# Performance work log

Hardware: AMD Instinct MI355X
Metric: run time of the kernel (lower is better)

## Reference

```python
import jax, jax.numpy as jnp
import numpy as np

DIM = 1024
HEADS = 16
SCALE = DIM ** -0.5  # NOTE: original uses full dim, not head dim


def setup_inputs() -> dict:
    key = jax.random.key(0)
    k1, k2, k3, k4 = jax.random.split(key, 4)
    x = jax.random.normal(k1, (2, 2048, DIM), dtype=jnp.float32)
    # torch nn.Linear(dim, 3*dim, bias=False): y = x @ W_qkv (stored here as [dim, 3*dim])
    w_qkv = jax.random.normal(k2, (DIM, 3 * DIM), dtype=jnp.float32) * (DIM ** -0.5)
    w_out = jax.random.normal(k3, (DIM, DIM), dtype=jnp.float32) * (DIM ** -0.5)
    b_out = jax.random.normal(k4, (DIM,), dtype=jnp.float32) * 0.01
    return {"x": x, "w_qkv": w_qkv, "w_out": w_out, "b_out": b_out}


def reference(x, w_qkv, w_out, b_out):
    b, n, d = x.shape
    h = HEADS
    hd = d // h
    qkv = x @ w_qkv  # [b, n, 3*d]
    # last dim layout is (qkv, h, hd) per rearrange 'b n (qkv h d) -> qkv b h n d'
    qkv = qkv.reshape(b, n, 3, h, hd)
    q, k, v = (jnp.moveaxis(qkv, (2, 3), (0, 2))[i] for i in range(3))  # each [b, h, n, hd]
    dots = jnp.einsum('bhid,bhjd->bhij', q, k) * SCALE
    causal_mask = jnp.triu(jnp.ones((n, n), dtype=bool), k=1)
    dots = jnp.where(causal_mask, -jnp.inf, dots)
    attn = jax.nn.softmax(dots, axis=-1)
    out = jnp.einsum('bhij,bhjd->bhid', attn, v)
    out = jnp.moveaxis(out, 1, 2).reshape(b, n, d)  # 'b h n d -> b n (h d)'
    return out @ w_out + b_out
```

## Files before the change

kernel.cpp:

```cpp
#include <hip/hip_runtime.h>

typedef __attribute__((ext_vector_type(8))) short bf16x8;
typedef __attribute__((ext_vector_type(4))) float f32x4;
typedef unsigned short u16;
typedef unsigned int u32;

#define SEQ 2048
#define NHEAD 16
#define EXP2_SCALE 0.045084219f

__device__ __forceinline__ u16 f2bf(float f){
  u32 u = __builtin_bit_cast(u32, f);
  u += 0x7FFFu + ((u >> 16) & 1u);
  return (u16)(u >> 16);
}

__device__ __forceinline__ void gl16(const u16* g, u16* l){
  __builtin_amdgcn_global_load_lds(
      (__attribute__((address_space(1))) void*)(unsigned long long)(const void*)g,
      (__attribute__((address_space(3))) void*)(unsigned)(unsigned long long)(const void*)l,
      16, 0, 0);
}

__global__ __launch_bounds__(256) void prep(const float* __restrict__ x,
                                            const float* __restrict__ w_qkv,
                                            const float* __restrict__ w_out,
                                            u16* __restrict__ xb,
                                            u16* __restrict__ wqkvT,
                                            u16* __restrict__ woutT){
  __shared__ u16 t[32][33];
  const int bid = blockIdx.x;
  if (bid < 4096){
    int i = (bid * 256 + threadIdx.x) << 2;
    float4 v = *(const float4*)&x[i];
    ushort4 o;
    o.x = f2bf(v.x); o.y = f2bf(v.y); o.z = f2bf(v.z); o.w = f2bf(v.w);
    *(ushort4*)&xb[i] = o;
    return;
  }
  const float* src; u16* dst; int R, C, bx, by;
  if (bid < 7168){ int tt = bid - 4096; src = w_qkv; dst = wqkvT; R = 1024; C = 3072; bx = tt % 96; by = tt / 96; }
  else           { int tt = bid - 7168; src = w_out; dst = woutT; R = 1024; C = 1024; bx = tt % 32; by = tt / 32; }
  const int c0 = bx << 5, r0 = by << 5;
  const int tx = threadIdx.x & 31, tg = threadIdx.x >> 5;
  #pragma unroll
  for (int i = 0; i < 4; i++){
    int r = (tg << 2) + i;
    t[r][tx] = f2bf(src[(size_t)(r0 + r) * C + (c0 + tx)]);
  }
  __syncthreads();
  #pragma unroll
  for (int i = 0; i < 4; i++){
    int c = (tg << 2) + i;
    dst[(size_t)(c0 + c) * R + (r0 + tx)] = t[tx][c];
  }
}

__device__ __forceinline__ int sw32(int row, int c){
  return row * 32 + (((c ^ ((row >> 1) & 3))) << 3);
}

__global__ __launch_bounds__(256) void gemm_qkv(const u16* __restrict__ A,
                                                const u16* __restrict__ Bt,
                                                u16* __restrict__ Qo,
                                                u16* __restrict__ Ko,
                                                u16* __restrict__ Vto){
  __shared__ u16 As[128 * 32];
  __shared__ u16 Bs[128 * 32];
  const int tid = threadIdx.x;
  const int lane = tid & 63, wid = tid >> 6;
  const int l15 = lane & 15, quad = lane >> 4;
  const int wm = wid >> 1, wn = wid & 1;
  const int bm = blockIdx.y << 7, bn = blockIdx.x << 7;
  const int qkv_idx = bn >> 10;

  const int rT = wid * 32 + (lane >> 2);
  const int cT = (lane & 3) ^ ((rT >> 1) & 3);
  const u16* gA0 = A  + (size_t)(bm + rT) * 1024 + cT * 8;
  const u16* gB0 = Bt + (size_t)(bn + rT) * 1024 + cT * 8;
  u16* lA0 = &As[wid * 1024];
  u16* lB0 = &Bs[wid * 1024];

  f32x4 acc[4][4];
  #pragma unroll
  for (int i = 0; i < 4; i++)
    #pragma unroll
    for (int j = 0; j < 4; j++) acc[i][j] = (f32x4){0.f, 0.f, 0.f, 0.f};

  if (qkv_idx != 2){
    for (int k0 = 0; k0 < 1024; k0 += 32){
      gl16(gA0 + k0,            lA0);
      gl16(gA0 + k0 + 16*1024,  lA0 + 512);
      gl16(gB0 + k0,            lB0);
      gl16(gB0 + k0 + 16*1024,  lB0 + 512);
      __syncthreads();
      bf16x8 af[4], bfr[4];
      #pragma unroll
      for (int mt = 0; mt < 4; mt++)
        af[mt] = *(const bf16x8*)&As[sw32(wm * 64 + mt * 16 + l15, quad)];
      #pragma unroll
      for (int nt = 0; nt < 4; nt++)
        bfr[nt] = *(const bf16x8*)&Bs[sw32(wn * 64 + nt * 16 + l15, quad)];
      #pragma unroll
      for (int mt = 0; mt < 4; mt++)
        #pragma unroll
        for (int nt = 0; nt < 4; nt++)
          acc[mt][nt] = __builtin_amdgcn_mfma_f32_16x16x32_bf16(af[mt], bfr[nt], acc[mt][nt], 0, 0, 0);
      __syncthreads();
    }
    const float qscale = (qkv_idx == 0) ? EXP2_SCALE : 1.0f;
    #pragma unroll
    for (int mt = 0; mt < 4; mt++){
      #pragma unroll
      for (int nt = 0; nt < 4; nt++){
        int col = bn + wn * 64 + nt * 16 + l15;
        int head = (col & 1023) >> 6, hd_i = col & 63;
        #pragma unroll
        for (int r = 0; r < 4; r++){
          int row = bm + wm * 64 + mt * 16 + quad * 4 + r;
          int b = row >> 11, pos = row & 2047;
          size_t bh = ((size_t)(b * NHEAD + head)) << 17;
          u16 v = f2bf(acc[mt][nt][r] * qscale);
          if (qkv_idx == 0) Qo[bh + ((size_t)pos << 6) + hd_i] = v;
          else              Ko[bh + ((size_t)pos << 6) + hd_i] = v;
        }
      }
    }
  } else {
    for (int k0 = 0; k0 < 1024; k0 += 32){
      gl16(gA0 + k0,            lA0);
      gl16(gA0 + k0 + 16*1024,  lA0 + 512);
      gl16(gB0 + k0,            lB0);
      gl16(gB0 + k0 + 16*1024,  lB0 + 512);
      __syncthreads();
      bf16x8 af[4], bfr[4];
      #pragma unroll
      for (int mt = 0; mt < 4; mt++)
        af[mt] = *(const bf16x8*)&As[sw32(wm * 64 + mt * 16 + l15, quad)];
      #pragma unroll
      for (int nt = 0; nt < 4; nt++)
        bfr[nt] = *(const bf16x8*)&Bs[sw32(wn * 64 + nt * 16 + l15, quad)];
      #pragma unroll
      for (int mt = 0; mt < 4; mt++)
        #pragma unroll
        for (int nt = 0; nt < 4; nt++)
          acc[mt][nt] = __builtin_amdgcn_mfma_f32_16x16x32_bf16(bfr[nt], af[mt], acc[mt][nt], 0, 0, 0);
      __syncthreads();
    }
    #pragma unroll
    for (int mt = 0; mt < 4; mt++){
      int row_m = bm + wm * 64 + mt * 16 + l15;
      int b = row_m >> 11, pos = row_m & 2047;
      #pragma unroll
      for (int nt = 0; nt < 4; nt++){
        #pragma unroll
        for (int r = 0; r < 4; r++){
          int c = bn + wn * 64 + nt * 16 + quad * 4 + r;
          int head = (c & 1023) >> 6, hd_i = c & 63;
          size_t bh = ((size_t)(b * NHEAD + head)) << 17;
          Vto[bh + ((size_t)hd_i << 11) + pos] = f2bf(acc[mt][nt][r]);
        }
      }
    }
  }
}

__global__ __launch_bounds__(256) void attn_kernel(const u16* __restrict__ Q,
                                                   const u16* __restrict__ K,
                                                   const u16* __restrict__ Vt,
                                                   u16* __restrict__ Oo){
  __shared__ u16 Ks[128 * 64];
  __shared__ u16 Vts[64 * 128];
  __shared__ u16 Ps[4][16 * 136];
  const int tid = threadIdx.x;
  const int lane = tid & 63, wid = tid >> 6;
  const int l15 = lane & 15, quad = lane >> 4;
  const int bh = blockIdx.x & 31;
  const int qt = 31 - (blockIdx.x >> 5);
  const size_t base = ((size_t)bh) << 17;
  const int b = bh >> 4, h = bh & 15;

  const u16* qsrc = Q + base + ((size_t)((qt << 6) + wid * 16 + l15) << 6) + quad * 8;
  const bf16x8 bq0 = *(const bf16x8*)qsrc;
  const bf16x8 bq1 = *(const bf16x8*)(qsrc + 32);

  const int rK = wid * 32 + (lane >> 3);
  const int cK = (lane & 7) ^ (rK & 7);
  const u16* gK0 = K + base + ((size_t)rK << 6) + cK * 8;
  u16* lK = &Ks[wid * 4 * 512];
  const u16* gV[4];
  #pragma unroll
  for (int t = 0; t < 4; t++){
    int rv = wid * 16 + t * 4 + (lane >> 4);
    int cv = (lane & 15) ^ (rv & 15);
    gV[t] = Vt + base + (size_t)rv * 2048 + cv * 8;
  }
  u16* lV = &Vts[wid * 4 * 512];

  f32x4 o[4];
  #pragma unroll
  for (int dt = 0; dt < 4; dt++) o[dt] = (f32x4){0.f, 0.f, 0.f, 0.f};
  float l = 0.f;
  const int qpos = (qt << 6) + wid * 16 + l15;
  const int jt_max = qt >> 1;
  u16* Pw = &Ps[wid][0];

  for (int jt = 0; jt <= jt_max; jt++){
    const u16* gk = gK0 + (size_t)jt * 8192;
    #pragma unroll
    for (int t = 0; t < 4; t++) gl16(gk + t * 512, lK + t * 512);
    #pragma unroll
    for (int t = 0; t < 4; t++) gl16(gV[t] + (jt << 7), lV + t * 512);
    __syncthreads();

    f32x4 st[8];
    #pragma unroll
    for (int mt = 0; mt < 8; mt++) st[mt] = (f32x4){0.f, 0.f, 0.f, 0.f};
    #pragma unroll
    for (int mt = 0; mt < 8; mt++){
      int kvr = mt * 16 + l15;
      bf16x8 ak0 = *(const bf16x8*)&Ks[kvr * 64 + ((quad ^ (kvr & 7)) << 3)];
      st[mt] = __builtin_amdgcn_mfma_f32_16x16x32_bf16(ak0, bq0, st[mt], 0, 0, 0);
      bf16x8 ak1 = *(const bf16x8*)&Ks[kvr * 64 + (((4 + quad) ^ (kvr & 7)) << 3)];
      st[mt] = __builtin_amdgcn_mfma_f32_16x16x32_bf16(ak1, bq1, st[mt], 0, 0, 0);
    }

    const bool diag = (jt == jt_max);
    float rs = 0.f;
    #pragma unroll
    for (int mt = 0; mt < 8; mt++){
      float pr[4];
      #pragma unroll
      for (int r = 0; r < 4; r++){
        float w = st[mt][r];
        if (diag){
          int kv = (jt << 7) + mt * 16 + quad * 4 + r;
          if (kv > qpos) w = -INFINITY;
        }
        pr[r] = __builtin_amdgcn_exp2f(w);
      }
      rs += (pr[0] + pr[1]) + (pr[2] + pr[3]);
      u32 a0 = __builtin_bit_cast(u32, pr[0]) + 0x8000u;
      u32 a1 = __builtin_bit_cast(u32, pr[1]) + 0x8000u;
      u32 a2 = __builtin_bit_cast(u32, pr[2]) + 0x8000u;
      u32 a3 = __builtin_bit_cast(u32, pr[3]) + 0x8000u;
      uint2 pk;
      pk.x = __builtin_amdgcn_perm(a1, a0, 0x07060302u);
      pk.y = __builtin_amdgcn_perm(a3, a2, 0x07060302u);
      *(uint2*)&Pw[l15 * 136 + mt * 16 + quad * 4] = pk;
    }
    rs += __shfl_xor(rs, 16);
    rs += __shfl_xor(rs, 32);
    l += rs;

    #pragma unroll
    for (int ks = 0; ks < 4; ks++){
      bf16x8 bp = *(const bf16x8*)&Pw[l15 * 136 + ks * 32 + quad * 8];
      #pragma unroll
      for (int dt = 0; dt < 4; dt++){
        int dr = dt * 16 + l15;
        bf16x8 av = *(const bf16x8*)&Vts[dr * 128 + (((ks * 4 + quad) ^ (dr & 15)) << 3)];
        o[dt] = __builtin_amdgcn_mfma_f32_16x16x32_bf16(av, bp, o[dt], 0, 0, 0);
      }
    }
    __syncthreads();
  }

  float inv = 1.f / l;
  const size_t orow = (size_t)((b << 11) + qpos) * 1024 + h * 64;
  #pragma unroll
  for (int dt = 0; dt < 4; dt++){
    ushort4 w;
    w.x = f2bf(o[dt][0] * inv); w.y = f2bf(o[dt][1] * inv);
    w.z = f2bf(o[dt][2] * inv); w.w = f2bf(o[dt][3] * inv);
    *(ushort4*)&Oo[orow + dt * 16 + quad * 4] = w;
  }
}

__global__ __launch_bounds__(256) void gemm_out(const u16* __restrict__ A,
                                                const u16* __restrict__ Bt,
                                                const float* __restrict__ bias,
                                                float* __restrict__ out){
  __shared__ u16 As[128 * 32];
  __shared__ u16 Bs[128 * 32];
  const int tid = threadIdx.x;
  const int lane = tid & 63, wid = tid >> 6;
  const int l15 = lane & 15, quad = lane >> 4;
  const int wm = wid >> 1, wn = wid & 1;
  const int bm = blockIdx.y << 7, bn = blockIdx.x << 7;

  const int rT = wid * 32 + (lane >> 2);
  const int cT = (lane & 3) ^ ((rT >> 1) & 3);
  const u16* gA0 = A  + (size_t)(bm + rT) * 1024 + cT * 8;
  const u16* gB0 = Bt + (size_t)(bn + rT) * 1024 + cT * 8;
  u16* lA0 = &As[wid * 1024];
  u16* lB0 = &Bs[wid * 1024];

  f32x4 acc[4][4];
  #pragma unroll
  for (int i = 0; i < 4; i++)
    #pragma unroll
    for (int j = 0; j < 4; j++) acc[i][j] = (f32x4){0.f, 0.f, 0.f, 0.f};

  for (int k0 = 0; k0 < 1024; k0 += 32){
    gl16(gA0 + k0,            lA0);
    gl16(gA0 + k0 + 16*1024,  lA0 + 512);
    gl16(gB0 + k0,            lB0);
    gl16(gB0 + k0 + 16*1024,  lB0 + 512);
    __syncthreads();

    bf16x8 af[4], bfr[4];
    #pragma unroll
    for (int mt = 0; mt < 4; mt++)
      af[mt] = *(const bf16x8*)&As[sw32(wm * 64 + mt * 16 + l15, quad)];
    #pragma unroll
    for (int nt = 0; nt < 4; nt++)
      bfr[nt] = *(const bf16x8*)&Bs[sw32(wn * 64 + nt * 16 + l15, quad)];
    #pragma unroll
    for (int mt = 0; mt < 4; mt++)
      #pragma unroll
      for (int nt = 0; nt < 4; nt++)
        acc[mt][nt] = __builtin_amdgcn_mfma_f32_16x16x32_bf16(af[mt], bfr[nt], acc[mt][nt], 0, 0, 0);
    __syncthreads();
  }

  #pragma unroll
  for (int nt = 0; nt < 4; nt++){
    int col = bn + wn * 64 + nt * 16 + l15;
    float bv = bias[col];
    #pragma unroll
    for (int mt = 0; mt < 4; mt++)
      #pragma unroll
      for (int r = 0; r < 4; r++){
        int row = bm + wm * 64 + mt * 16 + quad * 4 + r;
        out[(size_t)row * 1024 + col] = acc[mt][nt][r] + bv;
      }
  }
}

extern "C" void kernel_launch(void* const* d_in, const int* in_sizes, int n_in,
                              void* d_out, int out_size, void* d_ws, size_t ws_size,
                              hipStream_t stream){
  const float* x     = (const float*)d_in[0];
  const float* w_qkv = (const float*)d_in[1];
  const float* w_out = (const float*)d_in[2];
  const float* b_out = (const float*)d_in[3];
  float* out = (float*)d_out;

  char* ws = (char*)d_ws;
  u16* xb    = (u16*)(ws);
  u16* wqkvT = (u16*)(ws + (8u  << 20));
  u16* woutT = (u16*)(ws + (14u << 20));
  u16* Qb    = (u16*)(ws + (16u << 20));
  u16* Kb    = (u16*)(ws + (24u << 20));
  u16* Vtb   = (u16*)(ws + (32u << 20));
  u16* attn  = (u16*)(ws + (40u << 20));

  prep<<<8192, 256, 0, stream>>>(x, w_qkv, w_out, xb, wqkvT, woutT);
  gemm_qkv<<<dim3(24, 32), 256, 0, stream>>>(xb, wqkvT, Qb, Kb, Vtb);
  attn_kernel<<<dim3(1024), 256, 0, stream>>>(Qb, Kb, Vtb, attn);
  gemm_out<<<dim3(8, 32), 256, 0, stream>>>(attn, woutT, b_out, out);
}
```

Baseline: 177.6 us.

## Double GEMM K-tile to 64 and process two Q tiles per attention block

Both GEMMs now stage a 64-wide K slice per iteration with a new XOR swizzle. That halves the number of barriers and global-to-LDS rounds per output tile, and the two V-branch loops are merged into one. The attention kernel gives each block 128 query rows, as two 64-row sub-tiles, so each K/V tile loaded into LDS is reused twice, and it launches half as many blocks. In exchange, LDS use per GEMM block doubles, register pressure in attention rises, and attention has fewer blocks to spread across CUs, with coarser causal load balancing.

```diff
diff --git a/kernel.cpp b/kernel.cpp
--- a/kernel.cpp
+++ b/kernel.cpp
@@ -56,17 +56,13 @@
   }
 }
 
-__device__ __forceinline__ int sw32(int row, int c){
-  return row * 32 + (((c ^ ((row >> 1) & 3))) << 3);
-}
-
 __global__ __launch_bounds__(256) void gemm_qkv(const u16* __restrict__ A,
                                                 const u16* __restrict__ Bt,
                                                 u16* __restrict__ Qo,
                                                 u16* __restrict__ Ko,
                                                 u16* __restrict__ Vto){
-  __shared__ u16 As[128 * 32];
-  __shared__ u16 Bs[128 * 32];
+  __shared__ u16 As[128 * 64];
+  __shared__ u16 Bs[128 * 64];
   const int tid = threadIdx.x;
   const int lane = tid & 63, wid = tid >> 6;
   const int l15 = lane & 15, quad = lane >> 4;
@@ -74,12 +70,12 @@
   const int bm = blockIdx.y << 7, bn = blockIdx.x << 7;
   const int qkv_idx = bn >> 10;
 
-  const int rT = wid * 32 + (lane >> 2);
-  const int cT = (lane & 3) ^ ((rT >> 1) & 3);
-  const u16* gA0 = A  + (size_t)(bm + rT) * 1024 + cT * 8;
-  const u16* gB0 = Bt + (size_t)(bn + rT) * 1024 + cT * 8;
-  u16* lA0 = &As[wid * 1024];
-  u16* lB0 = &Bs[wid * 1024];
+  const int lr = lane >> 3;
+  const int cc = (lane & 7) ^ lr;
+  const u16* gA0 = A  + (size_t)(bm + wid * 32 + lr) * 1024 + (cc << 3);
+  const u16* gB0 = Bt + (size_t)(bn + wid * 32 + lr) * 1024 + (cc << 3);
+  u16* lA0 = &As[wid * 2048];
+  u16* lB0 = &Bs[wid * 2048];
 
   f32x4 acc[4][4];
   #pragma unroll
@@ -87,27 +83,45 @@
     #pragma unroll
     for (int j = 0; j < 4; j++) acc[i][j] = (f32x4){0.f, 0.f, 0.f, 0.f};
 
-  if (qkv_idx != 2){
-    for (int k0 = 0; k0 < 1024; k0 += 32){
-      gl16(gA0 + k0,            lA0);
-      gl16(gA0 + k0 + 16*1024,  lA0 + 512);
-      gl16(gB0 + k0,            lB0);
-      gl16(gB0 + k0 + 16*1024,  lB0 + 512);
-      __syncthreads();
+  const bool vbranch = (qkv_idx == 2);
+  for (int k0 = 0; k0 < 1024; k0 += 64){
+    #pragma unroll
+    for (int t = 0; t < 4; t++){
+      gl16(gA0 + k0 + t * 8192, lA0 + t * 512);
+      gl16(gB0 + k0 + t * 8192, lB0 + t * 512);
+    }
+    __syncthreads();
+    #pragma unroll
+    for (int hf = 0; hf < 2; hf++){
       bf16x8 af[4], bfr[4];
       #pragma unroll
-      for (int mt = 0; mt < 4; mt++)
-        af[mt] = *(const bf16x8*)&As[sw32(wm * 64 + mt * 16 + l15, quad)];
-      #pragma unroll
-      for (int nt = 0; nt < 4; nt++)
-        bfr[nt] = *(const bf16x8*)&Bs[sw32(wn * 64 + nt * 16 + l15, quad)];
-      #pragma unroll
-      for (int mt = 0; mt < 4; mt++)
-        #pragma unroll
-        for (int nt = 0; nt < 4; nt++)
-          acc[mt][nt] = __builtin_amdgcn_mfma_f32_16x16x32_bf16(af[mt], bfr[nt], acc[mt][nt], 0, 0, 0);
-      __syncthreads();
-    }
+      for (int mt = 0; mt < 4; mt++){
+        int row = wm * 64 + mt * 16 + l15;
+        af[mt] = *(const bf16x8*)&As[row * 64 + (((hf * 4 + quad) ^ (row & 7)) << 3)];
+      }
+      #pragma unroll
+      for (int nt = 0; nt < 4; nt++){
+        int row = wn * 64 + nt * 16 + l15;
+        bfr[nt] = *(const bf16x8*)&Bs[row * 64 + (((hf * 4 + quad) ^ (row & 7)) << 3)];
+      }
+      if (!vbranch){
+        #pragma unroll
+        for (int mt = 0; mt < 4; mt++)
+          #pragma unroll
+          for (int nt = 0; nt < 4; nt++)
+            acc[mt][nt] = __builtin_amdgcn_mfma_f32_16x16x32_bf16(af[mt], bfr[nt], acc[mt][nt], 0, 0, 0);
+      } else {
+        #pragma unroll
+        for (int mt = 0; mt < 4; mt++)
+          #pragma unroll
+          for (int nt = 0; nt < 4; nt++)
+            acc[mt][nt] = __builtin_amdgcn_mfma_f32_16x16x32_bf16(bfr[nt], af[mt], acc[mt][nt], 0, 0, 0);
+      }
+    }
+    __syncthreads();
+  }
+
+  if (!vbranch){
     const float qscale = (qkv_idx == 0) ? EXP2_SCALE : 1.0f;
     #pragma unroll
     for (int mt = 0; mt < 4; mt++){
@@ -127,26 +141,6 @@
       }
     }
   } else {
-    for (int k0 = 0; k0 < 1024; k0 += 32){
-      gl16(gA0 + k0,            lA0);
-      gl16(gA0 + k0 + 16*1024,  lA0 + 512);
-      gl16(gB0 + k0,            lB0);
-      gl16(gB0 + k0 + 16*1024,  lB0 + 512);
-      __syncthreads();
-      bf16x8 af[4], bfr[4];
-      #pragma unroll
-      for (int mt = 0; mt < 4; mt++)
-        af[mt] = *(const bf16x8*)&As[sw32(wm * 64 + mt * 16 + l15, quad)];
-      #pragma unroll
-      for (int nt = 0; nt < 4; nt++)
-        bfr[nt] = *(const bf16x8*)&Bs[sw32(wn * 64 + nt * 16 + l15, quad)];
-      #pragma unroll
-      for (int mt = 0; mt < 4; mt++)
-        #pragma unroll
-        for (int nt = 0; nt < 4; nt++)
-          acc[mt][nt] = __builtin_amdgcn_mfma_f32_16x16x32_bf16(bfr[nt], af[mt], acc[mt][nt], 0, 0, 0);
-      __syncthreads();
-    }
     #pragma unroll
     for (int mt = 0; mt < 4; mt++){
       int row_m = bm + wm * 64 + mt * 16 + l15;
@@ -176,33 +170,36 @@
   const int lane = tid & 63, wid = tid >> 6;
   const int l15 = lane & 15, quad = lane >> 4;
   const int bh = blockIdx.x & 31;
-  const int qt = 31 - (blockIdx.x >> 5);
+  const int qt2 = 15 - (blockIdx.x >> 5);
   const size_t base = ((size_t)bh) << 17;
   const int b = bh >> 4, h = bh & 15;
 
-  const u16* qsrc = Q + base + ((size_t)((qt << 6) + wid * 16 + l15) << 6) + quad * 8;
-  const bf16x8 bq0 = *(const bf16x8*)qsrc;
-  const bf16x8 bq1 = *(const bf16x8*)(qsrc + 32);
+  const u16* qsrc = Q + base + ((size_t)((qt2 << 7) + wid * 16 + l15) << 6) + quad * 8;
+  bf16x8 bq[2][2];
+  bq[0][0] = *(const bf16x8*)qsrc;
+  bq[0][1] = *(const bf16x8*)(qsrc + 32);
+  bq[1][0] = *(const bf16x8*)(qsrc + 4096);
+  bq[1][1] = *(const bf16x8*)(qsrc + 4096 + 32);
 
   const int rK = wid * 32 + (lane >> 3);
   const int cK = (lane & 7) ^ (rK & 7);
-  const u16* gK0 = K + base + ((size_t)rK << 6) + cK * 8;
-  u16* lK = &Ks[wid * 4 * 512];
+  const u16* gK0 = K + base + ((size_t)rK << 6) + (cK << 3);
+  u16* lK = &Ks[wid * 2048];
   const u16* gV[4];
   #pragma unroll
   for (int t = 0; t < 4; t++){
     int rv = wid * 16 + t * 4 + (lane >> 4);
     int cv = (lane & 15) ^ (rv & 15);
-    gV[t] = Vt + base + (size_t)rv * 2048 + cv * 8;
-  }
-  u16* lV = &Vts[wid * 4 * 512];
-
-  f32x4 o[4];
-  #pragma unroll
-  for (int dt = 0; dt < 4; dt++) o[dt] = (f32x4){0.f, 0.f, 0.f, 0.f};
-  float l = 0.f;
-  const int qpos = (qt << 6) + wid * 16 + l15;
-  const int jt_max = qt >> 1;
+    gV[t] = Vt + base + (size_t)rv * 2048 + (cv << 3);
+  }
+  u16* lV = &Vts[wid * 2048];
+
+  f32x4 o[8];
+  #pragma unroll
+  for (int i = 0; i < 8; i++) o[i] = (f32x4){0.f, 0.f, 0.f, 0.f};
+  float lsum[2] = {0.f, 0.f};
+  const int qp0 = (qt2 << 7) + wid * 16 + l15;
+  const int jt_max = qt2;
   u16* Pw = &Ps[wid][0];
 
   for (int jt = 0; jt <= jt_max; jt++){
@@ -213,67 +210,74 @@
     for (int t = 0; t < 4; t++) gl16(gV[t] + (jt << 7), lV + t * 512);
     __syncthreads();
 
-    f32x4 st[8];
-    #pragma unroll
-    for (int mt = 0; mt < 8; mt++) st[mt] = (f32x4){0.f, 0.f, 0.f, 0.f};
-    #pragma unroll
-    for (int mt = 0; mt < 8; mt++){
-      int kvr = mt * 16 + l15;
-      bf16x8 ak0 = *(const bf16x8*)&Ks[kvr * 64 + ((quad ^ (kvr & 7)) << 3)];
-      st[mt] = __builtin_amdgcn_mfma_f32_16x16x32_bf16(ak0, bq0, st[mt], 0, 0, 0);
-      bf16x8 ak1 = *(const bf16x8*)&Ks[kvr * 64 + (((4 + quad) ^ (kvr & 7)) << 3)];
-      st[mt] = __builtin_amdgcn_mfma_f32_16x16x32_bf16(ak1, bq1, st[mt], 0, 0, 0);
-    }
-
     const bool diag = (jt == jt_max);
-    float rs = 0.f;
-    #pragma unroll
-    for (int mt = 0; mt < 8; mt++){
-      float pr[4];
-      #pragma unroll
-      for (int r = 0; r < 4; r++){
-        float w = st[mt][r];
-        if (diag){
-          int kv = (jt << 7) + mt * 16 + quad * 4 + r;
-          if (kv > qpos) w = -INFINITY;
+    #pragma unroll
+    for (int s = 0; s < 2; s++){
+      f32x4 st[8];
+      #pragma unroll
+      for (int mt = 0; mt < 8; mt++) st[mt] = (f32x4){0.f, 0.f, 0.f, 0.f};
+      #pragma unroll
+      for (int mt = 0; mt < 8; mt++){
+        int kvr = mt * 16 + l15;
+        bf16x8 ak0 = *(const bf16x8*)&Ks[kvr * 64 + ((quad ^ (kvr & 7)) << 3)];
+        st[mt] = __builtin_amdgcn_mfma_f32_16x16x32_bf16(ak0, bq[s][0], st[mt], 0, 0, 0);
+        bf16x8 ak1 = *(const bf16x8*)&Ks[kvr * 64 + (((4 + quad) ^ (kvr & 7)) << 3)];
+        st[mt] = __builtin_amdgcn_mfma_f32_16x16x32_bf16(ak1, bq[s][1], st[mt], 0, 0, 0);
+      }
+
+      const int qpos = qp0 + s * 64;
+      float rs = 0.f;
+      #pragma unroll
+      for (int mt = 0; mt < 8; mt++){
+        float pr[4];
+        #pragma unroll
+        for (int r = 0; r < 4; r++){
+          float w = st[mt][r];
+          if (diag){
+            int kv = (jt << 7) + mt * 16 + quad * 4 + r;
+            if (kv > qpos) w = -INFINITY;
+          }
+          pr[r] = __builtin_amdgcn_exp2f(w);
         }
-        pr[r] = __builtin_amdgcn_exp2f(w);
-      }
-      rs += (pr[0] + pr[1]) + (pr[2] + pr[3]);
-      u32 a0 = __builtin_bit_cast(u32, pr[0]) + 0x8000u;
-      u32 a1 = __builtin_bit_cast(u32, pr[1]) + 0x8000u;
-      u32 a2 = __builtin_bit_cast(u32, pr[2]) + 0x8000u;
-      u32 a3 = __builtin_bit_cast(u32, pr[3]) + 0x8000u;
-      uint2 pk;
-      pk.x = __builtin_amdgcn_perm(a1, a0, 0x07060302u);
-      pk.y = __builtin_amdgcn_perm(a3, a2, 0x07060302u);
-      *(uint2*)&Pw[l15 * 136 + mt * 16 + quad * 4] = pk;
-    }
-    rs += __shfl_xor(rs, 16);
-    rs += __shfl_xor(rs, 32);
-    l += rs;
-
-    #pragma unroll
-    for (int ks = 0; ks < 4; ks++){
-      bf16x8 bp = *(const bf16x8*)&Pw[l15 * 136 + ks * 32 + quad * 8];
-      #pragma unroll
-      for (int dt = 0; dt < 4; dt++){
-        int dr = dt * 16 + l15;
-        bf16x8 av = *(const bf16x8*)&Vts[dr * 128 + (((ks * 4 + quad) ^ (dr & 15)) << 3)];
-        o[dt] = __builtin_amdgcn_mfma_f32_16x16x32_bf16(av, bp, o[dt], 0, 0, 0);
-      }
-    }
-    __syncthreads();
-  }
-
-  float inv = 1.f / l;
-  const size_t orow = (size_t)((b << 11) + qpos) * 1024 + h * 64;
-  #pragma unroll
-  for (int dt = 0; dt < 4; dt++){
-    ushort4 w;
-    w.x = f2bf(o[dt][0] * inv); w.y = f2bf(o[dt][1] * inv);
-    w.z = f2bf(o[dt][2] * inv); w.w = f2bf(o[dt][3] * inv);
-    *(ushort4*)&Oo[orow + dt * 16 + quad * 4] = w;
+        rs += (pr[0] + pr[1]) + (pr[2] + pr[3]);
+        u32 a0 = __builtin_bit_cast(u32, pr[0]) + 0x8000u;
+        u32 a1 = __builtin_bit_cast(u32, pr[1]) + 0x8000u;
+        u32 a2 = __builtin_bit_cast(u32, pr[2]) + 0x8000u;
+        u32 a3 = __builtin_bit_cast(u32, pr[3]) + 0x8000u;
+        uint2 pk;
+        pk.x = __builtin_amdgcn_perm(a1, a0, 0x07060302u);
+        pk.y = __builtin_amdgcn_perm(a3, a2, 0x07060302u);
+        *(uint2*)&Pw[l15 * 136 + mt * 16 + quad * 4] = pk;
+      }
+      rs += __shfl_xor(rs, 16);
+      rs += __shfl_xor(rs, 32);
+      lsum[s] += rs;
+
+      #pragma unroll
+      for (int ks = 0; ks < 4; ks++){
+        bf16x8 bp = *(const bf16x8*)&Pw[l15 * 136 + ks * 32 + quad * 8];
+        #pragma unroll
+        for (int dt = 0; dt < 4; dt++){
+          int dr = dt * 16 + l15;
+          bf16x8 av = *(const bf16x8*)&Vts[dr * 128 + (((ks * 4 + quad) ^ (dr & 15)) << 3)];
+          o[s * 4 + dt] = __builtin_amdgcn_mfma_f32_16x16x32_bf16(av, bp, o[s * 4 + dt], 0, 0, 0);
+        }
+      }
+    }
+    __syncthreads();
+  }
+
+  #pragma unroll
+  for (int s = 0; s < 2; s++){
+    float inv = 1.f / lsum[s];
+    const size_t orow = (size_t)((b << 11) + qp0 + s * 64) * 1024 + h * 64;
+    #pragma unroll
+    for (int dt = 0; dt < 4; dt++){
+      ushort4 w;
+      w.x = f2bf(o[s * 4 + dt][0] * inv); w.y = f2bf(o[s * 4 + dt][1] * inv);
+      w.z = f2bf(o[s * 4 + dt][2] * inv); w.w = f2bf(o[s * 4 + dt][3] * inv);
+      *(ushort4*)&Oo[orow + dt * 16 + quad * 4] = w;
+    }
   }
 }
 
@@ -281,20 +285,20 @@
                                                 const u16* __restrict__ Bt,
                                                 const float* __restrict__ bias,
                                                 float* __restrict__ out){
-  __shared__ u16 As[128 * 32];
-  __shared__ u16 Bs[128 * 32];
+  __shared__ u16 As[128 * 64];
+  __shared__ u16 Bs[128 * 64];
   const int tid = threadIdx.x;
   const int lane = tid & 63, wid = tid >> 6;
   const int l15 = lane & 15, quad = lane >> 4;
   const int wm = wid >> 1, wn = wid & 1;
   const int bm = blockIdx.y << 7, bn = blockIdx.x << 7;
 
-  const int rT = wid * 32 + (lane >> 2);
-  const int cT = (lane & 3) ^ ((rT >> 1) & 3);
-  const u16* gA0 = A  + (size_t)(bm + rT) * 1024 + cT * 8;
-  const u16* gB0 = Bt + (size_t)(bn + rT) * 1024 + cT * 8;
-  u16* lA0 = &As[wid * 1024];
-  u16* lB0 = &Bs[wid * 1024];
+  const int lr = lane >> 3;
+  const int cc = (lane & 7) ^ lr;
+  const u16* gA0 = A  + (size_t)(bm + wid * 32 + lr) * 1024 + (cc << 3);
+  const u16* gB0 = Bt + (size_t)(bn + wid * 32 + lr) * 1024 + (cc << 3);
+  u16* lA0 = &As[wid * 2048];
+  u16* lB0 = &Bs[wid * 2048];
 
   f32x4 acc[4][4];
   #pragma unroll
@@ -302,25 +306,32 @@
     #pragma unroll
     for (int j = 0; j < 4; j++) acc[i][j] = (f32x4){0.f, 0.f, 0.f, 0.f};
 
-  for (int k0 = 0; k0 < 1024; k0 += 32){
-    gl16(gA0 + k0,            lA0);
-    gl16(gA0 + k0 + 16*1024,  lA0 + 512);
-    gl16(gB0 + k0,            lB0);
-    gl16(gB0 + k0 + 16*1024,  lB0 + 512);
-    __syncthreads();
-
-    bf16x8 af[4], bfr[4];
-    #pragma unroll
-    for (int mt = 0; mt < 4; mt++)
-      af[mt] = *(const bf16x8*)&As[sw32(wm * 64 + mt * 16 + l15, quad)];
-    #pragma unroll
-    for (int nt = 0; nt < 4; nt++)
-      bfr[nt] = *(const bf16x8*)&Bs[sw32(wn * 64 + nt * 16 + l15, quad)];
-    #pragma unroll
-    for (int mt = 0; mt < 4; mt++)
-      #pragma unroll
-      for (int nt = 0; nt < 4; nt++)
-        acc[mt][nt] = __builtin_amdgcn_mfma_f32_16x16x32_bf16(af[mt], bfr[nt], acc[mt][nt], 0, 0, 0);
+  for (int k0 = 0; k0 < 1024; k0 += 64){
+    #pragma unroll
+    for (int t = 0; t < 4; t++){
+      gl16(gA0 + k0 + t * 8192, lA0 + t * 512);
+      gl16(gB0 + k0 + t * 8192, lB0 + t * 512);
+    }
+    __syncthreads();
+    #pragma unroll
+    for (int hf = 0; hf < 2; hf++){
+      bf16x8 af[4], bfr[4];
+      #pragma unroll
+      for (int mt = 0; mt < 4; mt++){
+        int row = wm * 64 + mt * 16 + l15;
+        af[mt] = *(const bf16x8*)&As[row * 64 + (((hf * 4 + quad) ^ (row & 7)) << 3)];
+      }
+      #pragma unroll
+      for (int nt = 0; nt < 4; nt++){
+        int row = wn * 64 + nt * 16 + l15;
+        bfr[nt] = *(const bf16x8*)&Bs[row * 64 + (((hf * 4 + quad) ^ (row & 7)) << 3)];
+      }
+      #pragma unroll
+      for (int mt = 0; mt < 4; mt++)
+        #pragma unroll
+        for (int nt = 0; nt < 4; nt++)
+          acc[mt][nt] = __builtin_amdgcn_mfma_f32_16x16x32_bf16(af[mt], bfr[nt], acc[mt][nt], 0, 0, 0);
+    }
     __syncthreads();
   }
 
@@ -358,6 +369,6 @@
 
   prep<<<8192, 256, 0, stream>>>(x, w_qkv, w_out, xb, wqkvT, woutT);
   gemm_qkv<<<dim3(24, 32), 256, 0, stream>>>(xb, wqkvT, Qb, Kb, Vtb);
-  attn_kernel<<<dim3(1024), 256, 0, stream>>>(Qb, Kb, Vtb, attn);
+  attn_kernel<<<dim3(512), 256, 0, stream>>>(Qb, Kb, Vtb, attn);
   gemm_out<<<dim3(8, 32), 256, 0, stream>>>(attn, woutT, b_out, out);
 }
```

Result: slower. 202.3 us (+13.9%).
